# Optimization experiments

Measured on AMD Instinct MI355X. Metric: run time of the kernel, lower is better.

Reference implementation:

```python
import jax, jax.numpy as jnp
import numpy as np

B, IN, OUT = 8192, 4096, 2048  # OUT must equal 32*64 per betta/gamma sizes


def setup_inputs() -> dict:
    key = jax.random.key(0)
    kx, kw = jax.random.split(key, 2)
    X = jax.random.normal(kx, (B, IN), dtype=jnp.float32)
    # xavier-uniform-like init for W
    limit = float(np.sqrt(6.0 / (IN + OUT)))
    W = jax.random.uniform(kw, (IN, OUT), minval=-limit, maxval=limit, dtype=jnp.float32)
    absmean = jnp.abs(W).mean(axis=0)
    alpha = jnp.abs(W).mean()          # scalar, >= 0
    betta = absmean[:32]               # (32,), >= 0
    gamma = absmean[32:96]             # (64,), >= 0
    return {"X": X, "W": W, "alpha": alpha, "betta": betta, "gamma": gamma}


def reference(X, W, alpha, betta, gamma):
    # module applies relu_ to alpha/betta/gamma data before the functional call
    alpha = jax.nn.relu(alpha)
    betta = jax.nn.relu(betta)
    gamma = jax.nn.relu(gamma)
    X_bin = jnp.sign(X)                # (B, IN)
    W_bin = jnp.sign(W)                # (IN, OUT)
    # scale[i*64+j] = alpha * betta[i] * gamma[j] -> (OUT,)
    scale = (alpha * jnp.outer(betta, gamma)).reshape(-1)
    return (X_bin @ W_bin) * scale     # (B, OUT)
```

## Files before the change

### kernel.cpp

```cpp
#include <hip/hip_runtime.h>


#define M_DIM 8192
#define K_DIM 4096
#define N_DIM 2048
#define NTK   (K_DIM / 128)
#define PANEL (128 * 128 * 16)
#define KSTEP 8192
#define BUFB  32768

typedef int i32x4 __attribute__((ext_vector_type(4)));
typedef int i32x8 __attribute__((ext_vector_type(8)));
typedef float f32x16 __attribute__((ext_vector_type(16)));

__device__ __forceinline__ unsigned int nib4(float x) {
  unsigned int s = (__float_as_uint(x) >> 28) & 0x8u;
  return x == 0.0f ? 0u : (0x2u | s);
}

__device__ __forceinline__ unsigned int pack8(const float* f) {
  unsigned int p = 0;
#pragma unroll
  for (int j = 0; j < 8; ++j) p |= nib4(f[j]) << (4 * j);
  return p;
}

__device__ __forceinline__ void gload_lds16(const void* g, void* lds) {
  __builtin_amdgcn_global_load_lds(
      (const __attribute__((address_space(1))) unsigned int*)g,
      (__attribute__((address_space(3))) unsigned int*)lds, 16, 0, 0);
}

__global__ __launch_bounds__(256) void binXW_kernel(
    const float* __restrict__ X, const float* __restrict__ W,
    unsigned char* __restrict__ Xq, unsigned char* __restrict__ Wq) {
  __shared__ float tile[32][260];
  const int t = threadIdx.x;
  const int bid = blockIdx.x;

  if (bid < 4096) {
    const int rg = bid >> 4;
    const int kc = bid & 15;
    const int lrow = t >> 6;
    const int col4 = (t & 63) * 4;
#pragma unroll
    for (int i = 0; i < 8; ++i)
      *(float4*)&tile[i * 4 + lrow][col4] =
          *(const float4*)&X[(size_t)(rg * 32 + i * 4 + lrow) * K_DIM + kc * 256 + col4];
    __syncthreads();
    const int s = t >> 5;
    const int r = t & 31;
    float f[32];
#pragma unroll
    for (int q = 0; q < 8; ++q)
      *(float4*)&f[q * 4] = *(const float4*)&tile[r][s * 32 + q * 4];
    uint4 gq;
    gq.x = pack8(f + 0);  gq.y = pack8(f + 8);
    gq.z = pack8(f + 16); gq.w = pack8(f + 24);
    const int row = rg * 32 + r;
    const int kslot = kc * 8 + s;
    unsigned char* dst = Xq + (size_t)(row >> 7) * PANEL +
                         ((size_t)kslot * 128 + (row & 127)) * 16;
    *(uint4*)dst = gq;
  } else {
    const int idx = bid - 4096;
    const int q = idx >> 7;
    const int kt = (idx >> 3) & 15;
    const int s = idx & 7;
#pragma unroll
    for (int i = 0; i < 8; ++i) {
      int row = i * 4 + (t >> 6);
      int col4 = (t & 63) * 4;
      *(float4*)&tile[row][col4] =
          *(const float4*)&W[(size_t)(kt * 256 + s * 32 + row) * N_DIM + q * 256 + col4];
    }
    __syncthreads();
    float f[32];
#pragma unroll
    for (int k = 0; k < 32; ++k) f[k] = tile[k][t];
    uint4 gq;
    gq.x = pack8(f + 0);  gq.y = pack8(f + 8);
    gq.z = pack8(f + 16); gq.w = pack8(f + 24);
    const int n = q * 256 + t;
    const int kslot = kt * 8 + s;
    unsigned char* dst = Wq + (size_t)(n >> 7) * PANEL +
                         ((size_t)kslot * 128 + (n & 127)) * 16;
    *(uint4*)dst = gq;
  }
}

__global__ __launch_bounds__(512, 2) void gemm_fp4_kernel(
    const unsigned char* __restrict__ Aq,
    const unsigned char* __restrict__ Bq,
    const float* __restrict__ alpha,
    const float* __restrict__ betta,
    const float* __restrict__ gamma,
    float* __restrict__ C) {
  __shared__ __align__(16) unsigned char smem[3 * BUFB];

  const int t = threadIdx.x;
  const int lane = t & 63;
  const int l31 = lane & 31;
  const int lhi = lane >> 5;
  const int w = t >> 6;
  const int wr = w >> 2;
  const int wc = w & 3;

  const int bid = blockIdx.x;
  const int j = bid >> 3;
  const int bm = (bid & 7) * 4 + (j & 3);
  const int bn = j >> 2;
  const int row0 = bm * 256;
  const int col0 = bn * 256;

  const unsigned char* Asrc0 = Aq + (size_t)(2 * bm) * PANEL;
  const unsigned char* Asrc1 = Asrc0 + PANEL;
  const unsigned char* Bsrc0 = Bq + (size_t)(2 * bn) * PANEL;
  const unsigned char* Bsrc1 = Bsrc0 + PANEL;

  f32x16 acc[4][2];
#pragma unroll
  for (int fm = 0; fm < 4; ++fm)
#pragma unroll
    for (int fn = 0; fn < 2; ++fn)
#pragma unroll
      for (int r = 0; r < 16; ++r) acc[fm][fn][r] = 0.f;

  i32x8 a8[4], b8[2];
#pragma unroll
  for (int i = 0; i < 4; ++i)
#pragma unroll
    for (int e = 0; e < 8; ++e) a8[i][e] = 0;
#pragma unroll
  for (int i = 0; i < 2; ++i)
#pragma unroll
    for (int e = 0; e < 8; ++e) b8[i][e] = 0;

  auto stage = [&](int kt, unsigned char* buf) {
    const size_t ko = (size_t)kt * KSTEP;
    gload_lds16(Asrc0 + ko + t * 16, buf + t * 16);
    gload_lds16(Asrc1 + ko + t * 16, buf + 8192 + t * 16);
    gload_lds16(Bsrc0 + ko + t * 16, buf + 16384 + t * 16);
    gload_lds16(Bsrc1 + ko + t * 16, buf + 24576 + t * 16);
  };

  auto compute = [&](const unsigned char* buf) {
    const unsigned char* pA = buf + wr * 8192;
    const unsigned char* pB = buf + 16384 + (wc >> 1) * 8192;
    const int cb = (wc & 1) * 64;
#pragma unroll
    for (int kk = 0; kk < 2; ++kk) {
      const int g = kk * 2 + lhi;
#pragma unroll
      for (int fm = 0; fm < 4; ++fm)
        *(i32x4*)&a8[fm] = *(const i32x4*)&pA[(g * 128 + fm * 32 + l31) * 16];
#pragma unroll
      for (int fn = 0; fn < 2; ++fn)
        *(i32x4*)&b8[fn] = *(const i32x4*)&pB[(g * 128 + cb + fn * 32 + l31) * 16];
      __builtin_amdgcn_s_setprio(1);
#pragma unroll
      for (int fm = 0; fm < 4; ++fm)
#pragma unroll
        for (int fn = 0; fn < 2; ++fn)
          acc[fm][fn] = __builtin_amdgcn_mfma_scale_f32_32x32x64_f8f6f4(
              a8[fm], b8[fn], acc[fm][fn], 4, 4,
              0, 0x7F7F7F7F, 0, 0x7F7F7F7F);
      __builtin_amdgcn_s_setprio(0);
    }
  };

  unsigned char* P0 = smem;
  unsigned char* P1 = smem + BUFB;
  unsigned char* P2 = smem + 2 * BUFB;

  stage(0, P0);
  stage(1, P1);

  for (int kt = 0; kt < NTK - 1; ++kt) {
    asm volatile("s_waitcnt vmcnt(4)" ::: "memory");
    __builtin_amdgcn_s_barrier();
    __builtin_amdgcn_sched_barrier(0);
    if (kt + 2 < NTK) stage(kt + 2, P2);
    compute(P0);
    unsigned char* tmp = P0; P0 = P1; P1 = P2; P2 = tmp;
  }
  asm volatile("s_waitcnt vmcnt(0)" ::: "memory");
  __builtin_amdgcn_s_barrier();
  __builtin_amdgcn_sched_barrier(0);
  compute(P0);

  const float ra = fmaxf(alpha[0], 0.0f);
#pragma unroll
  for (int fn = 0; fn < 2; ++fn) {
    const int col = col0 + wc * 64 + fn * 32 + l31;
    const float sc = ra * fmaxf(betta[col >> 6], 0.0f) * fmaxf(gamma[col & 63], 0.0f);
#pragma unroll
    for (int fm = 0; fm < 4; ++fm) {
      const int rbase = row0 + wr * 128 + fm * 32 + 4 * lhi;
#pragma unroll
      for (int r = 0; r < 16; ++r) {
        const int row = rbase + (r & 3) + 8 * (r >> 2);
        __builtin_nontemporal_store(acc[fm][fn][r] * sc,
                                    &C[(size_t)row * N_DIM + col]);
      }
    }
  }
}

extern "C" void kernel_launch(void* const* d_in, const int* in_sizes, int n_in,
                              void* d_out, int out_size, void* d_ws, size_t ws_size,
                              hipStream_t stream) {
  const float* X = (const float*)d_in[0];
  const float* W = (const float*)d_in[1];
  const float* alpha = (const float*)d_in[2];
  const float* betta = (const float*)d_in[3];
  const float* gamma = (const float*)d_in[4];
  float* out = (float*)d_out;

  unsigned char* Xq = (unsigned char*)d_ws;
  unsigned char* Wq = Xq + (size_t)(M_DIM / 128) * PANEL;

  binXW_kernel<<<5120, 256, 0, stream>>>(X, W, Xq, Wq);
  gemm_fp4_kernel<<<(M_DIM / 256) * (N_DIM / 256), 512, 0, stream>>>(
      Xq, Wq, alpha, betta, gamma, out);
}
```

Measured before the change: 70.98 us.

## Use 4 waves per GEMM block with larger per-wave 128x128 tiles

Halves the GEMM workgroup from 512 to 256 threads, so each wave now computes a 128x128 output sub-tile with a 4x4 MFMA fragment grid instead of 4x2. All LDS fragment loads for both k sub-steps are issued before the MFMA burst, and the setprio hints are removed. Each thread issues twice as many global-to-LDS loads, and the waitcnt threshold is raised to match. The intent is more operand reuse per LDS read and fewer waves contending, at the cost of doubled accumulator and operand registers, which forces lower occupancy (launch bounds 256,1).

```diff
diff --git a/kernel.cpp b/kernel.cpp
--- a/kernel.cpp
+++ b/kernel.cpp
@@ -89,7 +89,7 @@
   }
 }
 
-__global__ __launch_bounds__(512, 2) void gemm_fp4_kernel(
+__global__ __launch_bounds__(256, 1) void gemm_fp4_kernel(
     const unsigned char* __restrict__ Aq,
     const unsigned char* __restrict__ Bq,
     const float* __restrict__ alpha,
@@ -103,8 +103,8 @@
   const int l31 = lane & 31;
   const int lhi = lane >> 5;
   const int w = t >> 6;
-  const int wr = w >> 2;
-  const int wc = w & 3;
+  const int wr = w >> 1;
+  const int wc = w & 1;
 
   const int bid = blockIdx.x;
   const int j = bid >> 3;
@@ -118,55 +118,56 @@
   const unsigned char* Bsrc0 = Bq + (size_t)(2 * bn) * PANEL;
   const unsigned char* Bsrc1 = Bsrc0 + PANEL;
 
-  f32x16 acc[4][2];
+  f32x16 acc[4][4];
 #pragma unroll
   for (int fm = 0; fm < 4; ++fm)
 #pragma unroll
-    for (int fn = 0; fn < 2; ++fn)
+    for (int fn = 0; fn < 4; ++fn)
 #pragma unroll
       for (int r = 0; r < 16; ++r) acc[fm][fn][r] = 0.f;
 
-  i32x8 a8[4], b8[2];
-#pragma unroll
-  for (int i = 0; i < 4; ++i)
-#pragma unroll
-    for (int e = 0; e < 8; ++e) a8[i][e] = 0;
+  i32x8 a8[2][4], b8[2][4];
 #pragma unroll
   for (int i = 0; i < 2; ++i)
 #pragma unroll
-    for (int e = 0; e < 8; ++e) b8[i][e] = 0;
+    for (int q = 0; q < 4; ++q)
+#pragma unroll
+      for (int e = 0; e < 8; ++e) { a8[i][q][e] = 0; b8[i][q][e] = 0; }
 
   auto stage = [&](int kt, unsigned char* buf) {
     const size_t ko = (size_t)kt * KSTEP;
-    gload_lds16(Asrc0 + ko + t * 16, buf + t * 16);
-    gload_lds16(Asrc1 + ko + t * 16, buf + 8192 + t * 16);
-    gload_lds16(Bsrc0 + ko + t * 16, buf + 16384 + t * 16);
-    gload_lds16(Bsrc1 + ko + t * 16, buf + 24576 + t * 16);
+#pragma unroll
+    for (int p = 0; p < 2; ++p) {
+      const int c = (p * 256 + t) * 16;
+      gload_lds16(Asrc0 + ko + c, buf + c);
+      gload_lds16(Asrc1 + ko + c, buf + 8192 + c);
+      gload_lds16(Bsrc0 + ko + c, buf + 16384 + c);
+      gload_lds16(Bsrc1 + ko + c, buf + 24576 + c);
+    }
   };
 
   auto compute = [&](const unsigned char* buf) {
     const unsigned char* pA = buf + wr * 8192;
-    const unsigned char* pB = buf + 16384 + (wc >> 1) * 8192;
-    const int cb = (wc & 1) * 64;
+    const unsigned char* pB = buf + 16384 + wc * 8192;
 #pragma unroll
     for (int kk = 0; kk < 2; ++kk) {
       const int g = kk * 2 + lhi;
 #pragma unroll
       for (int fm = 0; fm < 4; ++fm)
-        *(i32x4*)&a8[fm] = *(const i32x4*)&pA[(g * 128 + fm * 32 + l31) * 16];
-#pragma unroll
-      for (int fn = 0; fn < 2; ++fn)
-        *(i32x4*)&b8[fn] = *(const i32x4*)&pB[(g * 128 + cb + fn * 32 + l31) * 16];
-      __builtin_amdgcn_s_setprio(1);
+        *(i32x4*)&a8[kk][fm] = *(const i32x4*)&pA[(g * 128 + fm * 32 + l31) * 16];
+#pragma unroll
+      for (int fn = 0; fn < 4; ++fn)
+        *(i32x4*)&b8[kk][fn] = *(const i32x4*)&pB[(g * 128 + fn * 32 + l31) * 16];
+    }
+#pragma unroll
+    for (int kk = 0; kk < 2; ++kk)
 #pragma unroll
       for (int fm = 0; fm < 4; ++fm)
 #pragma unroll
-        for (int fn = 0; fn < 2; ++fn)
+        for (int fn = 0; fn < 4; ++fn)
           acc[fm][fn] = __builtin_amdgcn_mfma_scale_f32_32x32x64_f8f6f4(
-              a8[fm], b8[fn], acc[fm][fn], 4, 4,
+              a8[kk][fm], b8[kk][fn], acc[fm][fn], 4, 4,
               0, 0x7F7F7F7F, 0, 0x7F7F7F7F);
-      __builtin_amdgcn_s_setprio(0);
-    }
   };
 
   unsigned char* P0 = smem;
@@ -177,7 +178,7 @@
   stage(1, P1);
 
   for (int kt = 0; kt < NTK - 1; ++kt) {
-    asm volatile("s_waitcnt vmcnt(4)" ::: "memory");
+    asm volatile("s_waitcnt vmcnt(8)" ::: "memory");
     __builtin_amdgcn_s_barrier();
     __builtin_amdgcn_sched_barrier(0);
     if (kt + 2 < NTK) stage(kt + 2, P2);
@@ -191,8 +192,8 @@
 
   const float ra = fmaxf(alpha[0], 0.0f);
 #pragma unroll
-  for (int fn = 0; fn < 2; ++fn) {
-    const int col = col0 + wc * 64 + fn * 32 + l31;
+  for (int fn = 0; fn < 4; ++fn) {
+    const int col = col0 + wc * 128 + fn * 32 + l31;
     const float sc = ra * fmaxf(betta[col >> 6], 0.0f) * fmaxf(gamma[col & 63], 0.0f);
 #pragma unroll
     for (int fm = 0; fm < 4; ++fm) {
@@ -221,6 +222,6 @@
   unsigned char* Wq = Xq + (size_t)(M_DIM / 128) * PANEL;
 
   binXW_kernel<<<5120, 256, 0, stream>>>(X, W, Xq, Wq);
-  gemm_fp4_kernel<<<(M_DIM / 256) * (N_DIM / 256), 512, 0, stream>>>(
+  gemm_fp4_kernel<<<(M_DIM / 256) * (N_DIM / 256), 256, 0, stream>>>(
       Xq, Wq, alpha, betta, gamma, out);
 }
```

Measured after the change: 74.24 us. 1.05x slower.
